# Kernel tuning notes

Hardware: AMD Instinct MI355X
Metric: run time of the kernel (lower is better)

The kernel has to match this reference:

```python
import jax, jax.numpy as jnp
import numpy as np

NUM_ORI = 16
DEGREE = 2
NUM_LAYERS = 2
LN_EPS = 1e-6


def ori_grid_s1(n):
    theta = jnp.linspace(0.0, 2.0 * jnp.pi, n + 1)[:-1]
    return jnp.stack([jnp.cos(theta), jnp.sin(theta)], axis=-1)  # (O, 2)


def poly_feats(z, degree):
    # PolynomialFeatures: [z, z*z outer, (z*z)*z outer ...] flattened
    feats = [z]
    p = z
    for _ in range(degree):
        p = (p[..., :, None] * z[..., None, :]).reshape(*z.shape[:-1], -1)
        feats.append(p)
    return jnp.concatenate(feats, axis=-1)


def basis_mlp(z, W1, b1, W2, b2):
    return jax.nn.gelu(jax.nn.gelu(z @ W1 + b1) @ W2 + b2)


def layer_norm(h, scale, bias):
    mu = h.mean(axis=-1, keepdims=True)
    var = ((h - mu) ** 2).mean(axis=-1, keepdims=True)
    return (h - mu) * jax.lax.rsqrt(var + LN_EPS) * scale + bias


def setup_inputs() -> dict:
    key = jax.random.key(0)
    ks = jax.random.split(key, 16)
    B, N, NIN, H, BD, WF, OUT, L = 1, 256, 3, 64, 32, 4, 3, NUM_LAYERS
    s = 0.05
    return {
        'pos': jax.random.normal(ks[0], (B, N, 2), jnp.float32),
        'x': jax.random.normal(ks[1], (B, N, NIN), jnp.float32),
        'skb_W1': jax.random.normal(ks[2], (14, H), jnp.float32) * s,
        'skb_b1': jnp.zeros((H,), jnp.float32),
        'skb_W2': jax.random.normal(ks[3], (H, BD), jnp.float32) * s,
        'skb_b2': jnp.zeros((BD,), jnp.float32),
        'rkb_W1': jax.random.normal(ks[4], (3, H), jnp.float32) * s,
        'rkb_b1': jnp.zeros((H,), jnp.float32),
        'rkb_W2': jax.random.normal(ks[5], (H, BD), jnp.float32) * s,
        'rkb_b2': jnp.zeros((BD,), jnp.float32),
        'emb_W': jax.random.normal(ks[6], (NIN, H), jnp.float32) * s,
        'conv_sW': jax.random.normal(ks[7], (L, BD, H), jnp.float32) * s,
        'conv_rW': jax.random.normal(ks[8], (L, BD, H), jnp.float32) * s,
        'conv_b': jnp.zeros((L, H), jnp.float32),
        'ln_scale': jnp.ones((L, H), jnp.float32),
        'ln_bias': jnp.zeros((L, H), jnp.float32),
        'lin1_W': jax.random.normal(ks[9], (L, H, WF * H), jnp.float32) * s,
        'lin1_b': jnp.zeros((L, WF * H), jnp.float32),
        'lin2_W': jax.random.normal(ks[10], (L, WF * H, H), jnp.float32) * s,
        'lin2_b': jnp.zeros((L, H), jnp.float32),
        'readout_W': jax.random.normal(ks[11], (H, OUT), jnp.float32) * s,
    }


def reference(pos, x, skb_W1, skb_b1, skb_W2, skb_b2, rkb_W1, rkb_b1, rkb_W2, rkb_b2,
              emb_W, conv_sW, conv_rW, conv_b, ln_scale, ln_bias,
              lin1_W, lin1_b, lin2_W, lin2_b, readout_W):
    ori = ori_grid_s1(NUM_ORI)  # (O, 2)
    # rel_pos: (B, n, m, 1, 2) -> broadcast against ori (O, 2)
    rel_pos = pos[:, None, :, None, :] - pos[:, :, None, None, :]
    inv1 = jnp.sum(rel_pos * ori[None, None, None, :, :], axis=-1, keepdims=True)  # (B,N,N,O,1)
    inv2 = jnp.linalg.norm(rel_pos - rel_pos * inv1, axis=-1, keepdims=True)       # (B,N,N,O,1)
    spatial_inv = jnp.concatenate([inv1, inv2], axis=-1)                            # (B,N,N,O,2)
    orient_inv = jnp.sum(ori[:, None, :] * ori[None, :, :], axis=-1, keepdims=True) # (O,O,1)

    kernel_basis = basis_mlp(poly_feats(spatial_inv, DEGREE), skb_W1, skb_b1, skb_W2, skb_b2)  # (B,N,N,O,BD)
    fiber_basis = basis_mlp(poly_feats(orient_inv, DEGREE), rkb_W1, rkb_b1, rkb_W2, rkb_b2)    # (O,O,BD)

    h = x @ emb_W                                  # (B,N,H)
    O = NUM_ORI
    h = jnp.broadcast_to(h[:, :, None, :], (h.shape[0], h.shape[1], O, h.shape[2]))  # (B,N,O,H)

    for i in range(NUM_LAYERS):
        inp = h
        sk = kernel_basis @ conv_sW[i]             # (B,N,N,O,H)
        rk = fiber_basis @ conv_rW[i]              # (O,O,H)
        c = jnp.einsum('bnoc,bmnoc->bmoc', h, sk)  # spatial aggregation
        c = jnp.einsum('bmoc,poc->bmpc', c, rk)    # orientation mixing
        c = c + conv_b[i]
        c = layer_norm(c, ln_scale[i], ln_bias[i])
        c = jax.nn.gelu(c @ lin1_W[i] + lin1_b[i]) @ lin2_W[i] + lin2_b[i]
        h = inp + c

    readout = h @ readout_W                        # (B,N,O,OUT)
    out_scalar = readout.mean(axis=-2)             # (B,N,OUT)
    out_scalar = jnp.sum(out_scalar, axis=1) / out_scalar.shape[1]  # global pool -> (B,OUT)
    return out_scalar
```

## Files before the change

kernel.cpp:

```cpp
#include <hip/hip_runtime.h>
#include <math.h>

#define NPTS 256
#define NORI 16
#define CH   64
#define BD   32
#define HID  64
#define STEP16 0.39269908169872414f

typedef __bf16 bf16x8 __attribute__((ext_vector_type(8)));
typedef float  f32x4  __attribute__((ext_vector_type(4)));

#define MFMA16(a, b, cc) __builtin_amdgcn_mfma_f32_16x16x32_bf16(a, b, cc, 0, 0, 0)

__device__ __forceinline__ float gelu_f(float x) {
    float x2 = x * x;
    float y2 = x * fmaf(0.07135481627f, x2, 1.5957691216f);
    float e = __expf(y2);
    return x - x * __builtin_amdgcn_rcpf(e + 1.0f);
}

__device__ __forceinline__ unsigned pk2(float x, float y) {
    union { __bf16 h[2]; unsigned u; } r;
    r.h[0] = (__bf16)x; r.h[1] = (__bf16)y;
    return r.u;
}

__device__ __forceinline__ void dev_prep(
    const float* __restrict__ skb_W1, const float* __restrict__ skb_W2,
    const float* __restrict__ conv_sW,
    __bf16* __restrict__ w1T, __bf16* __restrict__ w2T, __bf16* __restrict__ w2Tlo,
    __bf16* __restrict__ sWT, __bf16* __restrict__ sWTlo, int t)
{
    if (t < 64) {
        float f[9];
        f[0] = skb_W1[t];
        f[1] = skb_W1[64 + t];
        f[2] = skb_W1[128 + t];
        f[3] = skb_W1[192 + t] + skb_W1[256 + t];
        f[4] = skb_W1[320 + t];
        f[5] = skb_W1[384 + t];
        f[6] = skb_W1[448 + t] + skb_W1[512 + t] + skb_W1[640 + t];
        f[7] = skb_W1[576 + t] + skb_W1[704 + t] + skb_W1[768 + t];
        f[8] = skb_W1[832 + t];
#pragma unroll
        for (int k = 0; k < 9; ++k) {
            __bf16 hi = (__bf16)f[k];
            w1T[t * 32 + k]      = hi;
            w1T[t * 32 + 9 + k]  = (__bf16)(f[k] - (float)hi);
            w1T[t * 32 + 18 + k] = hi;
        }
#pragma unroll
        for (int k = 27; k < 32; ++k) w1T[t * 32 + k] = (__bf16)0.0f;
    }
    for (int i = t; i < 2048; i += 256) {
        int n = i >> 6, kk = i & 63;
        float v = skb_W2[kk * 32 + n];
        __bf16 hi = (__bf16)v;
        w2T[i]   = hi;
        w2Tlo[i] = (__bf16)(v - (float)hi);
    }
    for (int i = t; i < 4096; i += 256) {
        int ll = i >> 11, chh = (i >> 5) & 63, k = i & 31;
        float v = conv_sW[(ll * 32 + k) * 64 + chh];
        __bf16 hi = (__bf16)v;
        sWT[i]   = hi;
        sWTlo[i] = (__bf16)(v - (float)hi);
    }
}

__device__ __forceinline__ void dev_fiber(
    const float* __restrict__ rkb_W1, const float* __restrict__ rkb_b1,
    const float* __restrict__ rkb_W2, const float* __restrict__ rkb_b2,
    const float* __restrict__ conv_rW, float* __restrict__ rk, int p, int t)
{
    __shared__ float w1L[3 * 64], b1L[64], w2L[64 * 32], b2L[32];
    __shared__ float rwL[2 * 32 * 64];
    __shared__ float t1L[16 * 64];
    __shared__ float fbL[16 * 32];

    if (t < 192) w1L[t] = rkb_W1[t];
    if (t >= 192 && t < 256) b1L[t - 192] = rkb_b1[t - 192];
    for (int i = t; i < 2048; i += 256) w2L[i] = rkb_W2[i];
    if (t < 32) b2L[t] = rkb_b2[t];
    for (int i = t; i < 4096; i += 256) rwL[i] = conv_rW[i];
    __syncthreads();

    const int o = t & 15;
    const float cp = cosf(p * STEP16), sp = sinf(p * STEP16);
    const float co = cosf(o * STEP16), so = sinf(o * STEP16);
    const float s0 = cp * co + sp * so;
    const float m1 = s0 * s0, m2 = m1 * s0;

    {
        const int jg = t >> 4;
#pragma unroll
        for (int u = 0; u < 4; ++u) {
            const int j = jg * 4 + u;
            float a = b1L[j] + s0 * w1L[j] + m1 * w1L[64 + j] + m2 * w1L[128 + j];
            t1L[o * 64 + j] = gelu_f(a);
        }
    }
    __syncthreads();
    {
        const int kg = t >> 4;
#pragma unroll
        for (int kk = 0; kk < 2; ++kk) {
            const int k = kg + kk * 16;
            float a = b2L[k];
#pragma unroll
            for (int j = 0; j < 64; ++j) a += t1L[o * 64 + j] * w2L[j * 32 + k];
            fbL[o * 32 + k] = gelu_f(a);
        }
    }
    __syncthreads();
    {
        const int o2 = t >> 4;
        const int chg = (t & 15) * 4;
#pragma unroll
        for (int l = 0; l < 2; ++l) {
            f32x4 acc = {0.f, 0.f, 0.f, 0.f};
#pragma unroll
            for (int k = 0; k < 32; ++k) {
                const float fv = fbL[o2 * 32 + k];
                const f32x4 rv = *(const f32x4*)(rwL + (l * 32 + k) * 64 + chg);
                acc[0] = fmaf(fv, rv[0], acc[0]);
                acc[1] = fmaf(fv, rv[1], acc[1]);
                acc[2] = fmaf(fv, rv[2], acc[2]);
                acc[3] = fmaf(fv, rv[3], acc[3]);
            }
            *(f32x4*)(rk + (l * 256 + p * 16 + o2) * 64 + chg) = acc;
        }
    }
}

__global__ __launch_bounds__(256) void k_prep(
    const float* __restrict__ skb_W1, const float* __restrict__ skb_W2,
    const float* __restrict__ conv_sW,
    __bf16* __restrict__ w1T, __bf16* __restrict__ w2T, __bf16* __restrict__ w2Tlo,
    __bf16* __restrict__ sWT, __bf16* __restrict__ sWTlo)
{
    dev_prep(skb_W1, skb_W2, conv_sW, w1T, w2T, w2Tlo, sWT, sWTlo, threadIdx.x);
}

__global__ __launch_bounds__(256) void k_fiber2(
    const float* __restrict__ rkb_W1, const float* __restrict__ rkb_b1,
    const float* __restrict__ rkb_W2, const float* __restrict__ rkb_b2,
    const float* __restrict__ conv_rW, float* __restrict__ rk)
{
    dev_fiber(rkb_W1, rkb_b1, rkb_W2, rkb_b2, conv_rW, rk, blockIdx.x, threadIdx.x);
}

__global__ __launch_bounds__(256) void k_init(
    const float* __restrict__ x, const float* __restrict__ emb_W, float* __restrict__ h)
{
    int idx = blockIdx.x * 256 + threadIdx.x;
    int ch = idx & 63;
    int n  = idx >> 10;
    h[idx] = x[n * 3] * emb_W[ch] + x[n * 3 + 1] * emb_W[64 + ch] + x[n * 3 + 2] * emb_W[128 + ch];
}

__global__ __launch_bounds__(256) void k_setup(
    const float* __restrict__ x, const float* __restrict__ emb_W, float* __restrict__ h2,
    const float* __restrict__ rkb_W1, const float* __restrict__ rkb_b1,
    const float* __restrict__ rkb_W2, const float* __restrict__ rkb_b2,
    const float* __restrict__ conv_rW, float* __restrict__ rk,
    const float* __restrict__ skb_W1, const float* __restrict__ skb_W2,
    const float* __restrict__ conv_sW,
    __bf16* __restrict__ w1T, __bf16* __restrict__ w2T, __bf16* __restrict__ w2Tlo,
    __bf16* __restrict__ sWT, __bf16* __restrict__ sWTlo)
{
    const int b = blockIdx.x, t = threadIdx.x;
    if (b < 1024) {
        int idx = b * 256 + t;
        int ch = (idx >> 4) & 63;
        int n  = idx >> 10;
        h2[idx] = x[n * 3] * emb_W[ch] + x[n * 3 + 1] * emb_W[64 + ch]
                + x[n * 3 + 2] * emb_W[128 + ch];
    } else if (b < 1040) {
        dev_fiber(rkb_W1, rkb_b1, rkb_W2, rkb_b2, conv_rW, rk, b - 1024, t);
    } else {
        dev_prep(skb_W1, skb_W2, conv_sW, w1T, w2T, w2Tlo, sWT, sWTlo, t);
    }
}

__global__ __launch_bounds__(256) void k_kb2(
    const float* __restrict__ pos,
    const float* __restrict__ skb_b1, const float* __restrict__ skb_b2,
    const __bf16* __restrict__ w1T, const __bf16* __restrict__ w2T,
    const __bf16* __restrict__ w2Tlo, __bf16* __restrict__ kb_g)
{
    const int t = threadIdx.x;
    const int c = t & 15, qq = (t >> 4) & 3, w = t >> 6;
    const int pair = blockIdx.x >> 1, ohalf = blockIdx.x & 1;
    const int m0 = (pair >> 4) * 16, n0 = (pair & 15) * 16;

    bf16x8 w1B[4], w2A[2][2], w2Alo[2][2];
    float b1x[4][4], b2x[2][4];
#pragma unroll
    for (int ni = 0; ni < 4; ++ni) {
        w1B[ni] = *(const bf16x8*)(w1T + (ni * 16 + c) * 32 + qq * 8);
#pragma unroll
        for (int r = 0; r < 4; ++r) b1x[ni][r] = skb_b1[ni * 16 + qq * 4 + r];
    }
#pragma unroll
    for (int mk = 0; mk < 2; ++mk) {
#pragma unroll
        for (int ks = 0; ks < 2; ++ks) {
            w2A[mk][ks]   = *(const bf16x8*)(w2T   + (mk * 16 + c) * 64 + ks * 32 + qq * 8);
            w2Alo[mk][ks] = *(const bf16x8*)(w2Tlo + (mk * 16 + c) * 64 + ks * 32 + qq * 8);
        }
#pragma unroll
        for (int r = 0; r < 4; ++r) b2x[mk][r] = skb_b2[mk * 16 + qq * 4 + r];
    }

    const int n = n0 + c;
    const float pnx = pos[2 * n], pny = pos[2 * n + 1];
    float cosv[4], sinv[4];
#pragma unroll
    for (int oi = 0; oi < 4; ++oi) {
        float th = (float)(ohalf * 4 + oi) * STEP16;
        cosv[oi] = cosf(th); sinv[oi] = sinf(th);
    }
    const int s0lane = c + ((qq & 1) << 5);
    const int s1lane = s0lane + 16;
    const int selhi = qq >> 1;
    const f32x4 zf = {0.f, 0.f, 0.f, 0.f};

#pragma unroll 1
    for (int mi = 0; mi < 4; ++mi) {
        const int m = m0 + w * 4 + mi;
        const float dx = pnx - pos[2 * m];
        const float dy = pny - pos[2 * m + 1];
#pragma unroll
        for (int oi = 0; oi < 4; ++oi) {
            const int o = ohalf * 4 + oi;
            float a = dx * cosv[oi] + dy * sinv[oi];
            float vx = dx - dx * a, vy = dy - dy * a;
            float b = sqrtf(vx * vx + vy * vy);
            float mfv[9];
            mfv[0] = a; mfv[1] = b; mfv[2] = a * a; mfv[3] = a * b; mfv[4] = b * b;
            mfv[5] = mfv[2] * a; mfv[6] = mfv[2] * b; mfv[7] = mfv[3] * b; mfv[8] = mfv[4] * b;
            __bf16 mh[9], ml[9];
#pragma unroll
            for (int i = 0; i < 9; ++i) {
                mh[i] = (__bf16)mfv[i];
                ml[i] = (__bf16)(mfv[i] - (float)mh[i]);
            }
            bf16x8 mb;
            if (qq == 0) {
                mb[0]=mh[0]; mb[1]=mh[1]; mb[2]=mh[2]; mb[3]=mh[3];
                mb[4]=mh[4]; mb[5]=mh[5]; mb[6]=mh[6]; mb[7]=mh[7];
            } else if (qq == 1) {
                mb[0]=mh[8]; mb[1]=mh[0]; mb[2]=mh[1]; mb[3]=mh[2];
                mb[4]=mh[3]; mb[5]=mh[4]; mb[6]=mh[5]; mb[7]=mh[6];
            } else if (qq == 2) {
                mb[0]=mh[7]; mb[1]=mh[8]; mb[2]=ml[0]; mb[3]=ml[1];
                mb[4]=ml[2]; mb[5]=ml[3]; mb[6]=ml[4]; mb[7]=ml[5];
            } else {
                mb[0]=ml[6]; mb[1]=ml[7]; mb[2]=ml[8]; mb[3]=(__bf16)0.0f;
                mb[4]=(__bf16)0.0f; mb[5]=(__bf16)0.0f; mb[6]=(__bf16)0.0f; mb[7]=(__bf16)0.0f;
            }

            unsigned t1p[4][2];
#pragma unroll
            for (int ni = 0; ni < 4; ++ni) {
                f32x4 acc = MFMA16(w1B[ni], mb, zf);
                float g0 = gelu_f(acc[0] + b1x[ni][0]);
                float g1 = gelu_f(acc[1] + b1x[ni][1]);
                float g2 = gelu_f(acc[2] + b1x[ni][2]);
                float g3 = gelu_f(acc[3] + b1x[ni][3]);
                t1p[ni][0] = pk2(g0, g1);
                t1p[ni][1] = pk2(g2, g3);
            }

            bf16x8 B2[2];
#pragma unroll
            for (int ks = 0; ks < 2; ++ks) {
                const unsigned lo0 = t1p[ks * 2][0],     lo1 = t1p[ks * 2][1];
                const unsigned hi0 = t1p[ks * 2 + 1][0], hi1 = t1p[ks * 2 + 1][1];
                unsigned aL0 = (unsigned)__shfl((int)lo0, s0lane);
                unsigned aL1 = (unsigned)__shfl((int)lo1, s0lane);
                unsigned aL2 = (unsigned)__shfl((int)lo0, s1lane);
                unsigned aL3 = (unsigned)__shfl((int)lo1, s1lane);
                unsigned aH0 = (unsigned)__shfl((int)hi0, s0lane);
                unsigned aH1 = (unsigned)__shfl((int)hi1, s0lane);
                unsigned aH2 = (unsigned)__shfl((int)hi0, s1lane);
                unsigned aH3 = (unsigned)__shfl((int)hi1, s1lane);
                union { unsigned u[4]; bf16x8 v; } bu;
                bu.u[0] = selhi ? aH0 : aL0;
                bu.u[1] = selhi ? aH1 : aL1;
                bu.u[2] = selhi ? aH2 : aL2;
                bu.u[3] = selhi ? aH3 : aL3;
                B2[ks] = bu.v;
            }

            const size_t ptP = (size_t)((m * 256 + n) * 16 + o);
            const size_t ptM = (size_t)((n * 256 + m) * 16 + (o ^ 8));
#pragma unroll
            for (int mk = 0; mk < 2; ++mk) {
                f32x4 acc = MFMA16(w2A[mk][0], B2[0], zf);
                acc = MFMA16(w2A[mk][1], B2[1], acc);
                acc = MFMA16(w2Alo[mk][0], B2[0], acc);
                acc = MFMA16(w2Alo[mk][1], B2[1], acc);
                float g0 = gelu_f(acc[0] + b2x[mk][0]);
                float g1 = gelu_f(acc[1] + b2x[mk][1]);
                float g2 = gelu_f(acc[2] + b2x[mk][2]);
                float g3 = gelu_f(acc[3] + b2x[mk][3]);
                uint2 pv; pv.x = pk2(g0, g1); pv.y = pk2(g2, g3);
                const int off = mk * 32 + qq * 8;
                *(uint2*)((char*)kb_g + ptP * 64 + off) = pv;
                *(uint2*)((char*)kb_g + ptM * 64 + off) = pv;
            }
        }
    }
}

__global__ __launch_bounds__(512, 1) void k_conv(
    const __bf16* __restrict__ kb_g,
    const __bf16* __restrict__ sWT, const __bf16* __restrict__ sWTlo,
    const float* __restrict__ conv_b, const float* __restrict__ rkg,
    const float* __restrict__ ln_scale, const float* __restrict__ ln_bias,
    const float* __restrict__ lin1_W, const float* __restrict__ lin1_b,
    const float* __restrict__ lin2_W, const float* __restrict__ lin2_b,
    const float* __restrict__ h_in, float* __restrict__ h_out, int l)
{
    __shared__ __align__(16) unsigned char smem[57344];
    const int t = threadIdx.x;
    const int m = blockIdx.x;
    const int w = t >> 6, lane = t & 63;
    const int qq = lane >> 4, c = lane & 15;

    bf16x8 sWB[4], sWBlo[4];
#pragma unroll
    for (int ni = 0; ni < 4; ++ni) {
        sWB[ni]   = *(const bf16x8*)(sWT   + l * 2048 + (ni * 16 + c) * 32 + qq * 8);
        sWBlo[ni] = *(const bf16x8*)(sWTlo + l * 2048 + (ni * 16 + c) * 32 + qq * 8);
    }

    f32x4 cacc[4];
#pragma unroll
    for (int ni = 0; ni < 4; ++ni)
#pragma unroll
        for (int r = 0; r < 4; ++r) cacc[ni][r] = 0.f;

    const __bf16* kbm = kb_g + ((size_t)m << 17);

#pragma unroll 2
    for (int tile = 0; tile < 16; ++tile) {
#pragma unroll
        for (int mm = 0; mm < 2; ++mm) {
            const int mi = 2 * w + mm;
            const int n = tile * 16 + mi;
            bf16x8 aF = *(const bf16x8*)(kbm + (size_t)(tile * 256 + mi * 16 + c) * 32 + qq * 8);
#pragma unroll
            for (int ni = 0; ni < 4; ++ni) {
                f32x4 g3 = {0.f, 0.f, 0.f, 0.f};
                g3 = MFMA16(aF, sWB[ni], g3);
                g3 = MFMA16(aF, sWBlo[ni], g3);
                f32x4 hv = *(const f32x4*)(h_in + n * 1024 + (ni * 16 + c) * 16 + qq * 4);
#pragma unroll
                for (int r = 0; r < 4; ++r) cacc[ni][r] = fmaf(g3[r], hv[r], cacc[ni][r]);
            }
        }
    }

    {
        float* c1p = (float*)smem;
#pragma unroll
        for (int ni = 0; ni < 4; ++ni)
#pragma unroll
            for (int r = 0; r < 4; ++r)
                c1p[w * 1024 + (qq * 4 + r) * 64 + ni * 16 + c] = cacc[ni][r];
    }
    __syncthreads();
    {
        float* c1p = (float*)smem;
        float* c1r = (float*)(smem + 32768);
        for (int i = t; i < 1024; i += 512) {
            float s = 0.f;
#pragma unroll
            for (int ww = 0; ww < 8; ++ww) s += c1p[ww * 1024 + i];
            c1r[i] = s;
        }
    }
    __syncthreads();

    {
        float* c1r = (float*)(smem + 32768);
        float* cns = (float*)(smem + 36864);
        const int ch = lane;
        const float cb  = conv_b[l * 64 + ch];
        const float lsc = ln_scale[l * 64 + ch], lbi = ln_bias[l * 64 + ch];
#pragma unroll
        for (int pp = 0; pp < 2; ++pp) {
            const int p = w + pp * 8;
            const float* rkp = rkg + (l * 256 + p * 16) * 64 + ch;
            float s = cb;
#pragma unroll
            for (int o = 0; o < 16; ++o) s += c1r[o * 64 + ch] * rkp[o * 64];
            float red = s;
#pragma unroll
            for (int off = 32; off > 0; off >>= 1) red += __shfl_xor(red, off);
            float mu = red * (1.0f / 64.0f);
            float d = s - mu;
            float r2 = d * d;
#pragma unroll
            for (int off = 32; off > 0; off >>= 1) r2 += __shfl_xor(r2, off);
            cns[p * 64 + ch] = d * rsqrtf(r2 * (1.0f / 64.0f) + 1e-6f) * lsc + lbi;
        }
    }
    __syncthreads();

    {
        float* cns = (float*)(smem + 36864);
        float* usS = (float*)(smem + 40960);
        const int j = t & 255, half = t >> 8;
        const float* W1l = lin1_W + l * 64 * 256;
        const float bl1 = lin1_b[l * 256 + j];
        float ua[8];
#pragma unroll
        for (int pi = 0; pi < 8; ++pi) ua[pi] = bl1;
#pragma unroll 4
        for (int c2 = 0; c2 < 64; ++c2) {
            const float wv = W1l[c2 * 256 + j];
#pragma unroll
            for (int pi = 0; pi < 8; ++pi)
                ua[pi] = fmaf(cns[(half * 8 + pi) * 64 + c2], wv, ua[pi]);
        }
#pragma unroll
        for (int pi = 0; pi < 8; ++pi) usS[(half * 8 + pi) * 256 + j] = gelu_f(ua[pi]);
    }
    __syncthreads();

    {
        float* usS = (float*)(smem + 40960);
        const int ch2 = t & 63, pg = t >> 6;
        const float* W2l = lin2_W + l * 256 * 64;
        const float bl2 = lin2_b[l * 64 + ch2];
        float o0 = bl2, o1 = bl2;
#pragma unroll 4
        for (int j = 0; j < 256; ++j) {
            const float wv = W2l[j * 64 + ch2];
            o0 = fmaf(usS[pg * 256 + j], wv, o0);
            o1 = fmaf(usS[(pg + 8) * 256 + j], wv, o1);
        }
        const int i0 = m * 1024 + ch2 * 16 + pg;
        h_out[i0]     = h_in[i0]     + o0;
        h_out[i0 + 8] = h_in[i0 + 8] + o1;
    }
}

__global__ __launch_bounds__(512, 1) void k_layer2(
    const float* __restrict__ pos,
    const float* __restrict__ skb_b1, const float* __restrict__ skb_b2,
    const __bf16* __restrict__ w1T, const __bf16* __restrict__ w2T,
    const __bf16* __restrict__ w2Tlo,
    const __bf16* __restrict__ sWT, const __bf16* __restrict__ sWTlo,
    const float* __restrict__ conv_b, const float* __restrict__ rkg,
    const float* __restrict__ ln_scale, const float* __restrict__ ln_bias,
    const float* __restrict__ lin1_W, const float* __restrict__ lin1_b,
    const float* __restrict__ lin2_W, const float* __restrict__ lin2_b,
    const float* __restrict__ h_in, float* __restrict__ h_out, int l)
{
    __shared__ __align__(16) unsigned char smem[57344];
    const int t = threadIdx.x;
    const int m = blockIdx.x;
    const int w = t >> 6, lane = t & 63;
    const int qq = lane >> 4, c = lane & 15;

    bf16x8 w1B[4], sWB[4], sWBlo[4], w2B[2][2], w2Blo[2][2];
    float b1v[4], b2v[2];
#pragma unroll
    for (int ni = 0; ni < 4; ++ni) {
        w1B[ni]   = *(const bf16x8*)(w1T + (ni * 16 + c) * 32 + qq * 8);
        sWB[ni]   = *(const bf16x8*)(sWT   + l * 2048 + (ni * 16 + c) * 32 + qq * 8);
        sWBlo[ni] = *(const bf16x8*)(sWTlo + l * 2048 + (ni * 16 + c) * 32 + qq * 8);
        b1v[ni] = skb_b1[ni * 16 + c];
    }
#pragma unroll
    for (int nt = 0; nt < 2; ++nt) {
        b2v[nt] = skb_b2[nt * 16 + c];
#pragma unroll
        for (int ks = 0; ks < 2; ++ks) {
            w2B[nt][ks]   = *(const bf16x8*)(w2T   + (nt * 16 + c) * 64 + ks * 32 + qq * 8);
            w2Blo[nt][ks] = *(const bf16x8*)(w2Tlo + (nt * 16 + c) * 64 + ks * 32 + qq * 8);
        }
    }

    const float pmx = pos[2 * m], pmy = pos[2 * m + 1];
    float co_ = 0.f, so_ = 0.f;
    if (t < 256) { float th = (float)(t & 15) * STEP16; co_ = cosf(th); so_ = sinf(th); }

    f32x4 cacc[4];
#pragma unroll
    for (int ni = 0; ni < 4; ++ni)
#pragma unroll
        for (int r = 0; r < 4; ++r) cacc[ni][r] = 0.f;

#pragma unroll 1
    for (int tile = 0; tile < 16; ++tile) {
        if (t < 256) {
            const int n = tile * 16 + (t >> 4);
            float dx = pos[2 * n] - pmx, dy = pos[2 * n + 1] - pmy;
            float a = dx * co_ + dy * so_;
            float vx = dx - dx * a, vy = dy - dy * a;
            float b = sqrtf(vx * vx + vy * vy);
            float mf[9];
            mf[0] = a; mf[1] = b; mf[2] = a * a; mf[3] = a * b; mf[4] = b * b;
            mf[5] = mf[2] * a; mf[6] = mf[2] * b; mf[7] = mf[3] * b; mf[8] = mf[4] * b;
            __bf16 s[32];
#pragma unroll
            for (int i = 0; i < 9; ++i) {
                __bf16 hi = (__bf16)mf[i];
                s[i] = hi; s[9 + i] = hi;
                s[18 + i] = (__bf16)(mf[i] - (float)hi);
            }
#pragma unroll
            for (int i = 27; i < 32; ++i) s[i] = (__bf16)0.0f;
            unsigned char* rowp = smem + t * 64;
#pragma unroll
            for (int u = 0; u < 4; ++u) {
                bf16x8 vv;
#pragma unroll
                for (int j = 0; j < 8; ++j) vv[j] = s[u * 8 + j];
                *(bf16x8*)(rowp + ((u ^ (t & 3)) << 4)) = vv;
            }
        }
        __syncthreads();

#pragma unroll
        for (int mm = 0; mm < 2; ++mm) {
            const int row = (2 * w + mm) * 16 + c;
            bf16x8 aF = *(const bf16x8*)(smem + row * 64 + ((qq ^ (row & 3)) << 4));
#pragma unroll
            for (int ni = 0; ni < 4; ++ni) {
                f32x4 acc = {0.f, 0.f, 0.f, 0.f};
                acc = MFMA16(aF, w1B[ni], acc);
#pragma unroll
                for (int r = 0; r < 4; ++r) {
                    const int ro = (2 * w + mm) * 16 + qq * 4 + r;
                    float g = gelu_f(acc[r] + b1v[ni]);
                    const int chc = ni * 16 + c;
                    *(__bf16*)(smem + 16384 + ro * 128 + (((chc >> 3) ^ (ro & 7)) << 4)
                               + ((chc & 7) << 1)) = (__bf16)g;
                }
            }
        }
        __syncthreads();

#pragma unroll
        for (int mm = 0; mm < 2; ++mm) {
            const int row = (2 * w + mm) * 16 + c;
            bf16x8 a0 = *(const bf16x8*)(smem + 16384 + row * 128 + ((qq ^ (row & 7)) << 4));
            bf16x8 a1 = *(const bf16x8*)(smem + 16384 + row * 128 + (((4 + qq) ^ (row & 7)) << 4));
#pragma unroll
            for (int nt = 0; nt < 2; ++nt) {
                f32x4 acc = {0.f, 0.f, 0.f, 0.f};
                acc = MFMA16(a0, w2B[nt][0], acc);
                acc = MFMA16(a1, w2B[nt][1], acc);
                acc = MFMA16(a0, w2Blo[nt][0], acc);
                acc = MFMA16(a1, w2Blo[nt][1], acc);
#pragma unroll
                for (int r = 0; r < 4; ++r) {
                    const int ro = (2 * w + mm) * 16 + qq * 4 + r;
                    float g = gelu_f(acc[r] + b2v[nt]);
                    const int kc = nt * 16 + c;
                    *(__bf16*)(smem + ro * 64 + (((kc >> 3) ^ (ro & 3)) << 4)
                               + ((kc & 7) << 1)) = (__bf16)g;
                }
            }
        }
        __syncthreads();

#pragma unroll
        for (int mm = 0; mm < 2; ++mm) {
            const int mi = 2 * w + mm;
            const int row = mi * 16 + c;
            bf16x8 aF = *(const bf16x8*)(smem + row * 64 + ((qq ^ (row & 3)) << 4));
            const int nbase = (tile * 16 + mi) * 1024 + qq * 256;
#pragma unroll
            for (int ni = 0; ni < 4; ++ni) {
                f32x4 g3 = {0.f, 0.f, 0.f, 0.f};
                g3 = MFMA16(aF, sWB[ni], g3);
                g3 = MFMA16(aF, sWBlo[ni], g3);
#pragma unroll
                for (int r = 0; r < 4; ++r) {
                    float hv = h_in[nbase + r * 64 + ni * 16 + c];
                    cacc[ni][r] = fmaf(g3[r], hv, cacc[ni][r]);
                }
            }
        }
        __syncthreads();
    }

    {
        float* c1p = (float*)smem;
#pragma unroll
        for (int ni = 0; ni < 4; ++ni)
#pragma unroll
            for (int r = 0; r < 4; ++r)
                c1p[w * 1024 + (qq * 4 + r) * 64 + ni * 16 + c] = cacc[ni][r];
    }
    __syncthreads();
    {
        float* c1p = (float*)smem;
        float* c1r = (float*)(smem + 32768);
        for (int i = t; i < 1024; i += 512) {
            float s = 0.f;
#pragma unroll
            for (int ww = 0; ww < 8; ++ww) s += c1p[ww * 1024 + i];
            c1r[i] = s;
        }
    }
    __syncthreads();

    {
        float* c1r = (float*)(smem + 32768);
        float* cns = (float*)(smem + 36864);
        const int ch = lane;
        const float cb  = conv_b[l * 64 + ch];
        const float lsc = ln_scale[l * 64 + ch], lbi = ln_bias[l * 64 + ch];
#pragma unroll
        for (int pp = 0; pp < 2; ++pp) {
            const int p = w + pp * 8;
            const float* rkp = rkg + (l * 256 + p * 16) * 64 + ch;
            float s = cb;
#pragma unroll
            for (int o = 0; o < 16; ++o) s += c1r[o * 64 + ch] * rkp[o * 64];
            float red = s;
#pragma unroll
            for (int off = 32; off > 0; off >>= 1) red += __shfl_xor(red, off);
            float mu = red * (1.0f / 64.0f);
            float d = s - mu;
            float r2 = d * d;
#pragma unroll
            for (int off = 32; off > 0; off >>= 1) r2 += __shfl_xor(r2, off);
            cns[p * 64 + ch] = d * rsqrtf(r2 * (1.0f / 64.0f) + 1e-6f) * lsc + lbi;
        }
    }
    __syncthreads();

    {
        float* cns = (float*)(smem + 36864);
        float* usS = (float*)(smem + 40960);
        const int j = t & 255, half = t >> 8;
        const float* W1l = lin1_W + l * 64 * 256;
        const float bl1 = lin1_b[l * 256 + j];
        float ua[8];
#pragma unroll
        for (int pi = 0; pi < 8; ++pi) ua[pi] = bl1;
#pragma unroll 1
        for (int c2 = 0; c2 < 64; ++c2) {
            const float wv = W1l[c2 * 256 + j];
#pragma unroll
            for (int pi = 0; pi < 8; ++pi)
                ua[pi] = fmaf(cns[(half * 8 + pi) * 64 + c2], wv, ua[pi]);
        }
#pragma unroll
        for (int pi = 0; pi < 8; ++pi) usS[(half * 8 + pi) * 256 + j] = gelu_f(ua[pi]);
    }
    __syncthreads();

    {
        float* usS = (float*)(smem + 40960);
        const int ch2 = t & 63, pg = t >> 6;
        const float* W2l = lin2_W + l * 256 * 64;
        const float bl2 = lin2_b[l * 64 + ch2];
        float o0 = bl2, o1 = bl2;
#pragma unroll 2
        for (int j = 0; j < 256; ++j) {
            const float wv = W2l[j * 64 + ch2];
            o0 = fmaf(usS[pg * 256 + j], wv, o0);
            o1 = fmaf(usS[(pg + 8) * 256 + j], wv, o1);
        }
        const int i0 = (m * 16 + pg) * 64 + ch2;
        const int i1 = (m * 16 + pg + 8) * 64 + ch2;
        h_out[i0] = h_in[i0] + o0;
        h_out[i1] = h_in[i1] + o1;
    }
}

__global__ __launch_bounds__(256) void k_readout_part(
    const float* __restrict__ h, float* __restrict__ part16)
{
    __shared__ float part[4][64];
    const int t = threadIdx.x, b = blockIdx.x;
    const int c = t & 63, seg = t >> 6;
    float s = 0.f;
    const int r0 = b * 256 + seg * 64;
    for (int r = r0; r < r0 + 64; ++r) s += h[r * 64 + c];
    part[seg][c] = s;
    __syncthreads();
    if (t < 64) part16[b * 64 + t] = part[0][t] + part[1][t] + part[2][t] + part[3][t];
}

__global__ __launch_bounds__(256) void k_readout_part2(
    const float* __restrict__ h, float* __restrict__ part16)
{
    const int t = threadIdx.x, b = blockIdx.x;
    const int ch = t >> 2, oq = t & 3;
    float s = 0.f;
#pragma unroll
    for (int nn = 0; nn < 16; ++nn) {
        const int n = b * 16 + nn;
        f32x4 v = *(const f32x4*)(h + n * 1024 + ch * 16 + oq * 4);
        s += (v[0] + v[1]) + (v[2] + v[3]);
    }
    s += __shfl_xor(s, 1);
    s += __shfl_xor(s, 2);
    if (oq == 0) part16[b * 64 + ch] = s;
}

__global__ __launch_bounds__(64) void k_readout_final(
    const float* __restrict__ part16, const float* __restrict__ rW, float* __restrict__ out)
{
    __shared__ float hbar[64];
    const int t = threadIdx.x;
    float s = 0.f;
#pragma unroll
    for (int b = 0; b < 16; ++b) s += part16[b * 64 + t];
    hbar[t] = s * (1.0f / 4096.0f);
    __syncthreads();
    if (t < 3) {
        float s2 = 0.f;
#pragma unroll
        for (int k = 0; k < 64; ++k) s2 += hbar[k] * rW[k * 3 + t];
        out[t] = s2;
    }
}

extern "C" void kernel_launch(void* const* d_in, const int* in_sizes, int n_in,
                              void* d_out, int out_size, void* d_ws, size_t ws_size,
                              hipStream_t stream)
{
    const float* pos      = (const float*)d_in[0];
    const float* x        = (const float*)d_in[1];
    const float* skb_W1   = (const float*)d_in[2];
    const float* skb_b1   = (const float*)d_in[3];
    const float* skb_W2   = (const float*)d_in[4];
    const float* skb_b2   = (const float*)d_in[5];
    const float* rkb_W1   = (const float*)d_in[6];
    const float* rkb_b1   = (const float*)d_in[7];
    const float* rkb_W2   = (const float*)d_in[8];
    const float* rkb_b2   = (const float*)d_in[9];
    const float* emb_W    = (const float*)d_in[10];
    const float* conv_sW  = (const float*)d_in[11];
    const float* conv_rW  = (const float*)d_in[12];
    const float* conv_b   = (const float*)d_in[13];
    const float* ln_scale = (const float*)d_in[14];
    const float* ln_bias  = (const float*)d_in[15];
    const float* lin1_W   = (const float*)d_in[16];
    const float* lin1_b   = (const float*)d_in[17];
    const float* lin2_W   = (const float*)d_in[18];
    const float* lin2_b   = (const float*)d_in[19];
    const float* readout_W= (const float*)d_in[20];
    float* out = (float*)d_out;

    unsigned char* ws = (unsigned char*)d_ws;
    float*  h_a    = (float*)(ws);
    float*  h_b    = (float*)(ws + 1048576);
    float*  rkw    = (float*)(ws + 2097152);
    __bf16* w1T    = (__bf16*)(ws + 2228224);
    __bf16* w2T    = (__bf16*)(ws + 2232320);
    __bf16* w2Tlo  = (__bf16*)(ws + 2236416);
    __bf16* sWT    = (__bf16*)(ws + 2240512);
    __bf16* sWTlo  = (__bf16*)(ws + 2248704);
    float*  part16 = (float*)(ws + 2256896);
    __bf16* kb_g   = (__bf16*)(ws + 2260992);

    const bool fast = (ws_size >= 2260992ull + 67108864ull);

    if (fast) {
        k_setup<<<1041, 256, 0, stream>>>(x, emb_W, h_a,
                                          rkb_W1, rkb_b1, rkb_W2, rkb_b2, conv_rW, rkw,
                                          skb_W1, skb_W2, conv_sW,
                                          w1T, w2T, w2Tlo, sWT, sWTlo);
        k_kb2<<<512, 256, 0, stream>>>(pos, skb_b1, skb_b2, w1T, w2T, w2Tlo, kb_g);
        k_conv<<<256, 512, 0, stream>>>(kb_g, sWT, sWTlo, conv_b, rkw,
                                        ln_scale, ln_bias, lin1_W, lin1_b,
                                        lin2_W, lin2_b, h_a, h_b, 0);
        k_conv<<<256, 512, 0, stream>>>(kb_g, sWT, sWTlo, conv_b, rkw,
                                        ln_scale, ln_bias, lin1_W, lin1_b,
                                        lin2_W, lin2_b, h_b, h_a, 1);
        k_readout_part2<<<16, 256, 0, stream>>>(h_a, part16);
        k_readout_final<<<1, 64, 0, stream>>>(part16, readout_W, out);
    } else {
        k_prep<<<1, 256, 0, stream>>>(skb_W1, skb_W2, conv_sW, w1T, w2T, w2Tlo, sWT, sWTlo);
        k_fiber2<<<16, 256, 0, stream>>>(rkb_W1, rkb_b1, rkb_W2, rkb_b2, conv_rW, rkw);
        k_init<<<1024, 256, 0, stream>>>(x, emb_W, h_a);
        k_layer2<<<256, 512, 0, stream>>>(pos, skb_b1, skb_b2, w1T, w2T, w2Tlo, sWT, sWTlo,
                                          conv_b, rkw, ln_scale, ln_bias, lin1_W, lin1_b,
                                          lin2_W, lin2_b, h_a, h_b, 0);
        k_layer2<<<256, 512, 0, stream>>>(pos, skb_b1, skb_b2, w1T, w2T, w2Tlo, sWT, sWTlo,
                                          conv_b, rkw, ln_scale, ln_bias, lin1_W, lin1_b,
                                          lin2_W, lin2_b, h_b, h_a, 1);
        k_readout_part<<<16, 256, 0, stream>>>(h_a, part16);
        k_readout_final<<<1, 64, 0, stream>>>(part16, readout_W, out);
    }
}
```

Baseline: 157.2 us.

## Double block size of conv kernel and software-prefetch next tile operands

```diff
diff --git a/kernel.cpp b/kernel.cpp
--- a/kernel.cpp
+++ b/kernel.cpp
@@ -316,7 +316,7 @@
     }
 }
 
-__global__ __launch_bounds__(512, 1) void k_conv(
+__global__ __launch_bounds__(1024) void k_conv2(
     const __bf16* __restrict__ kb_g,
     const __bf16* __restrict__ sWT, const __bf16* __restrict__ sWTlo,
     const float* __restrict__ conv_b, const float* __restrict__ rkg,
@@ -325,11 +325,12 @@
     const float* __restrict__ lin2_W, const float* __restrict__ lin2_b,
     const float* __restrict__ h_in, float* __restrict__ h_out, int l)
 {
-    __shared__ __align__(16) unsigned char smem[57344];
+    __shared__ __align__(16) unsigned char smem[90112];
     const int t = threadIdx.x;
     const int m = blockIdx.x;
     const int w = t >> 6, lane = t & 63;
     const int qq = lane >> 4, c = lane & 15;
+    const f32x4 zf = {0.f, 0.f, 0.f, 0.f};
 
     bf16x8 sWB[4], sWBlo[4];
 #pragma unroll
@@ -345,24 +346,48 @@
         for (int r = 0; r < 4; ++r) cacc[ni][r] = 0.f;
 
     const __bf16* kbm = kb_g + ((size_t)m << 17);
-
-#pragma unroll 2
+    const __bf16* abase = kbm + (size_t)(w * 16 + c) * 32 + qq * 8;
+
+    bf16x8 aF = *(const bf16x8*)(abase);
+    f32x4 hc0, hc1, hc2, hc3;
+    {
+        const float* hp = h_in + (w) * 1024 + c * 16 + qq * 4;
+        hc0 = *(const f32x4*)(hp);
+        hc1 = *(const f32x4*)(hp + 256);
+        hc2 = *(const f32x4*)(hp + 512);
+        hc3 = *(const f32x4*)(hp + 768);
+    }
+
+#pragma unroll 1
     for (int tile = 0; tile < 16; ++tile) {
-#pragma unroll
-        for (int mm = 0; mm < 2; ++mm) {
-            const int mi = 2 * w + mm;
-            const int n = tile * 16 + mi;
-            bf16x8 aF = *(const bf16x8*)(kbm + (size_t)(tile * 256 + mi * 16 + c) * 32 + qq * 8);
-#pragma unroll
-            for (int ni = 0; ni < 4; ++ni) {
-                f32x4 g3 = {0.f, 0.f, 0.f, 0.f};
-                g3 = MFMA16(aF, sWB[ni], g3);
-                g3 = MFMA16(aF, sWBlo[ni], g3);
-                f32x4 hv = *(const f32x4*)(h_in + n * 1024 + (ni * 16 + c) * 16 + qq * 4);
-#pragma unroll
-                for (int r = 0; r < 4; ++r) cacc[ni][r] = fmaf(g3[r], hv[r], cacc[ni][r]);
-            }
-        }
+        const int tn = (tile < 15) ? tile + 1 : 15;
+        bf16x8 aN = *(const bf16x8*)(abase + (size_t)tn * 8192);
+        const float* hpn = h_in + (tn * 16 + w) * 1024 + c * 16 + qq * 4;
+        f32x4 hn0 = *(const f32x4*)(hpn);
+        f32x4 hn1 = *(const f32x4*)(hpn + 256);
+        f32x4 hn2 = *(const f32x4*)(hpn + 512);
+        f32x4 hn3 = *(const f32x4*)(hpn + 768);
+
+        f32x4 g;
+        g = MFMA16(aF, sWB[0], zf);
+        g = MFMA16(aF, sWBlo[0], g);
+#pragma unroll
+        for (int r = 0; r < 4; ++r) cacc[0][r] = fmaf(g[r], hc0[r], cacc[0][r]);
+        g = MFMA16(aF, sWB[1], zf);
+        g = MFMA16(aF, sWBlo[1], g);
+#pragma unroll
+        for (int r = 0; r < 4; ++r) cacc[1][r] = fmaf(g[r], hc1[r], cacc[1][r]);
+        g = MFMA16(aF, sWB[2], zf);
+        g = MFMA16(aF, sWBlo[2], g);
+#pragma unroll
+        for (int r = 0; r < 4; ++r) cacc[2][r] = fmaf(g[r], hc2[r], cacc[2][r]);
+        g = MFMA16(aF, sWB[3], zf);
+        g = MFMA16(aF, sWBlo[3], g);
+#pragma unroll
+        for (int r = 0; r < 4; ++r) cacc[3][r] = fmaf(g[r], hc3[r], cacc[3][r]);
+
+        aF = aN;
+        hc0 = hn0; hc1 = hn1; hc2 = hn2; hc3 = hn3;
     }
 
     {
@@ -376,78 +401,67 @@
     __syncthreads();
     {
         float* c1p = (float*)smem;
-        float* c1r = (float*)(smem + 32768);
-        for (int i = t; i < 1024; i += 512) {
-            float s = 0.f;
-#pragma unroll
-            for (int ww = 0; ww < 8; ++ww) s += c1p[ww * 1024 + i];
-            c1r[i] = s;
-        }
-    }
-    __syncthreads();
-
-    {
-        float* c1r = (float*)(smem + 32768);
-        float* cns = (float*)(smem + 36864);
+        float* c1r = (float*)(smem + 65536);
+        float s = 0.f;
+#pragma unroll
+        for (int ww = 0; ww < 16; ++ww) s += c1p[ww * 1024 + t];
+        c1r[t] = s;
+    }
+    __syncthreads();
+
+    {
+        float* c1r = (float*)(smem + 65536);
+        float* cns = (float*)(smem + 69632);
         const int ch = lane;
         const float cb  = conv_b[l * 64 + ch];
         const float lsc = ln_scale[l * 64 + ch], lbi = ln_bias[l * 64 + ch];
-#pragma unroll
-        for (int pp = 0; pp < 2; ++pp) {
-            const int p = w + pp * 8;
-            const float* rkp = rkg + (l * 256 + p * 16) * 64 + ch;
-            float s = cb;
-#pragma unroll
-            for (int o = 0; o < 16; ++o) s += c1r[o * 64 + ch] * rkp[o * 64];
-            float red = s;
-#pragma unroll
-            for (int off = 32; off > 0; off >>= 1) red += __shfl_xor(red, off);
-            float mu = red * (1.0f / 64.0f);
-            float d = s - mu;
-            float r2 = d * d;
-#pragma unroll
-            for (int off = 32; off > 0; off >>= 1) r2 += __shfl_xor(r2, off);
-            cns[p * 64 + ch] = d * rsqrtf(r2 * (1.0f / 64.0f) + 1e-6f) * lsc + lbi;
-        }
-    }
-    __syncthreads();
-
-    {
-        float* cns = (float*)(smem + 36864);
-        float* usS = (float*)(smem + 40960);
-        const int j = t & 255, half = t >> 8;
+        const float* rkp = rkg + (l * 256 + w * 16) * 64 + ch;
+        float s = cb;
+#pragma unroll
+        for (int o = 0; o < 16; ++o) s += c1r[o * 64 + ch] * rkp[o * 64];
+        float red = s;
+#pragma unroll
+        for (int off = 32; off > 0; off >>= 1) red += __shfl_xor(red, off);
+        float mu = red * (1.0f / 64.0f);
+        float d = s - mu;
+        float r2 = d * d;
+#pragma unroll
+        for (int off = 32; off > 0; off >>= 1) r2 += __shfl_xor(r2, off);
+        cns[w * 64 + ch] = d * rsqrtf(r2 * (1.0f / 64.0f) + 1e-6f) * lsc + lbi;
+    }
+    __syncthreads();
+
+    {
+        float* cns = (float*)(smem + 69632);
+        float* usS = (float*)(smem + 73728);
+        const int j = t & 255, q4 = t >> 8;
         const float* W1l = lin1_W + l * 64 * 256;
         const float bl1 = lin1_b[l * 256 + j];
-        float ua[8];
-#pragma unroll
-        for (int pi = 0; pi < 8; ++pi) ua[pi] = bl1;
+        float ua[4];
+#pragma unroll
+        for (int pi = 0; pi < 4; ++pi) ua[pi] = bl1;
 #pragma unroll 4
         for (int c2 = 0; c2 < 64; ++c2) {
             const float wv = W1l[c2 * 256 + j];
 #pragma unroll
-            for (int pi = 0; pi < 8; ++pi)
-                ua[pi] = fmaf(cns[(half * 8 + pi) * 64 + c2], wv, ua[pi]);
-        }
-#pragma unroll
-        for (int pi = 0; pi < 8; ++pi) usS[(half * 8 + pi) * 256 + j] = gelu_f(ua[pi]);
-    }
-    __syncthreads();
-
-    {
-        float* usS = (float*)(smem + 40960);
+            for (int pi = 0; pi < 4; ++pi)
+                ua[pi] = fmaf(cns[(q4 * 4 + pi) * 64 + c2], wv, ua[pi]);
+        }
+#pragma unroll
+        for (int pi = 0; pi < 4; ++pi) usS[(q4 * 4 + pi) * 256 + j] = gelu_f(ua[pi]);
+    }
+    __syncthreads();
+
+    {
+        float* usS = (float*)(smem + 73728);
         const int ch2 = t & 63, pg = t >> 6;
         const float* W2l = lin2_W + l * 256 * 64;
-        const float bl2 = lin2_b[l * 64 + ch2];
-        float o0 = bl2, o1 = bl2;
+        float o0 = lin2_b[l * 64 + ch2];
 #pragma unroll 4
-        for (int j = 0; j < 256; ++j) {
-            const float wv = W2l[j * 64 + ch2];
-            o0 = fmaf(usS[pg * 256 + j], wv, o0);
-            o1 = fmaf(usS[(pg + 8) * 256 + j], wv, o1);
-        }
+        for (int j = 0; j < 256; ++j)
+            o0 = fmaf(usS[pg * 256 + j], W2l[j * 64 + ch2], o0);
         const int i0 = m * 1024 + ch2 * 16 + pg;
-        h_out[i0]     = h_in[i0]     + o0;
-        h_out[i0 + 8] = h_in[i0 + 8] + o1;
+        h_out[i0] = h_in[i0] + o0;
     }
 }
 
@@ -777,12 +791,12 @@
                                           skb_W1, skb_W2, conv_sW,
                                           w1T, w2T, w2Tlo, sWT, sWTlo);
         k_kb2<<<512, 256, 0, stream>>>(pos, skb_b1, skb_b2, w1T, w2T, w2Tlo, kb_g);
-        k_conv<<<256, 512, 0, stream>>>(kb_g, sWT, sWTlo, conv_b, rkw,
-                                        ln_scale, ln_bias, lin1_W, lin1_b,
-                                        lin2_W, lin2_b, h_a, h_b, 0);
-        k_conv<<<256, 512, 0, stream>>>(kb_g, sWT, sWTlo, conv_b, rkw,
-                                        ln_scale, ln_bias, lin1_W, lin1_b,
-                                        lin2_W, lin2_b, h_b, h_a, 1);
+        k_conv2<<<256, 1024, 0, stream>>>(kb_g, sWT, sWTlo, conv_b, rkw,
+                                          ln_scale, ln_bias, lin1_W, lin1_b,
+                                          lin2_W, lin2_b, h_a, h_b, 0);
+        k_conv2<<<256, 1024, 0, stream>>>(kb_g, sWT, sWTlo, conv_b, rkw,
+                                          ln_scale, ln_bias, lin1_W, lin1_b,
+                                          lin2_W, lin2_b, h_b, h_a, 1);
         k_readout_part2<<<16, 256, 0, stream>>>(h_a, part16);
         k_readout_final<<<1, 64, 0, stream>>>(part16, readout_W, out);
     } else {
```

Result: faster. 146.3 us (-6.9%).

## Fuse kernel-basis MLP into conv kernel, recompute per layer instead of materialising

Applied to the files above, without the earlier changes.

```diff
diff --git a/kernel.cpp b/kernel.cpp
--- a/kernel.cpp
+++ b/kernel.cpp
@@ -27,9 +27,10 @@
 }
 
 __device__ __forceinline__ void dev_prep(
-    const float* __restrict__ skb_W1, const float* __restrict__ skb_W2,
-    const float* __restrict__ conv_sW,
+    const float* __restrict__ skb_W1, const float* __restrict__ skb_b1,
+    const float* __restrict__ skb_W2, const float* __restrict__ conv_sW,
     __bf16* __restrict__ w1T, __bf16* __restrict__ w2T, __bf16* __restrict__ w2Tlo,
+    __bf16* __restrict__ w2Tp, __bf16* __restrict__ w2Tplo,
     __bf16* __restrict__ sWT, __bf16* __restrict__ sWTlo, int t)
 {
     if (t < 64) {
@@ -52,6 +53,10 @@
         }
 #pragma unroll
         for (int k = 27; k < 32; ++k) w1T[t * 32 + k] = (__bf16)0.0f;
+        float bv = skb_b1[t];
+        __bf16 bh = (__bf16)bv;
+        w1T[t * 32 + 27] = bh;
+        w1T[t * 32 + 28] = (__bf16)(bv - (float)bh);
     }
     for (int i = t; i < 2048; i += 256) {
         int n = i >> 6, kk = i & 63;
@@ -59,6 +64,13 @@
         __bf16 hi = (__bf16)v;
         w2T[i]   = hi;
         w2Tlo[i] = (__bf16)(v - (float)hi);
+        int row = i >> 6, ch = i & 63;
+        int mk = row >> 4, ii = row & 15;
+        int kp = 8 * (ii >> 2) + 4 * mk + (ii & 3);
+        float vp = skb_W2[ch * 32 + kp];
+        __bf16 hp = (__bf16)vp;
+        w2Tp[i]   = hp;
+        w2Tplo[i] = (__bf16)(vp - (float)hp);
     }
     for (int i = t; i < 4096; i += 256) {
         int ll = i >> 11, chh = (i >> 5) & 63, k = i & 31;
@@ -135,12 +147,14 @@
 }
 
 __global__ __launch_bounds__(256) void k_prep(
-    const float* __restrict__ skb_W1, const float* __restrict__ skb_W2,
-    const float* __restrict__ conv_sW,
+    const float* __restrict__ skb_W1, const float* __restrict__ skb_b1,
+    const float* __restrict__ skb_W2, const float* __restrict__ conv_sW,
     __bf16* __restrict__ w1T, __bf16* __restrict__ w2T, __bf16* __restrict__ w2Tlo,
+    __bf16* __restrict__ w2Tp, __bf16* __restrict__ w2Tplo,
     __bf16* __restrict__ sWT, __bf16* __restrict__ sWTlo)
 {
-    dev_prep(skb_W1, skb_W2, conv_sW, w1T, w2T, w2Tlo, sWT, sWTlo, threadIdx.x);
+    dev_prep(skb_W1, skb_b1, skb_W2, conv_sW, w1T, w2T, w2Tlo, w2Tp, w2Tplo,
+             sWT, sWTlo, threadIdx.x);
 }
 
 __global__ __launch_bounds__(256) void k_fiber2(
@@ -165,9 +179,10 @@
     const float* __restrict__ rkb_W1, const float* __restrict__ rkb_b1,
     const float* __restrict__ rkb_W2, const float* __restrict__ rkb_b2,
     const float* __restrict__ conv_rW, float* __restrict__ rk,
-    const float* __restrict__ skb_W1, const float* __restrict__ skb_W2,
-    const float* __restrict__ conv_sW,
+    const float* __restrict__ skb_W1, const float* __restrict__ skb_b1,
+    const float* __restrict__ skb_W2, const float* __restrict__ conv_sW,
     __bf16* __restrict__ w1T, __bf16* __restrict__ w2T, __bf16* __restrict__ w2Tlo,
+    __bf16* __restrict__ w2Tp, __bf16* __restrict__ w2Tplo,
     __bf16* __restrict__ sWT, __bf16* __restrict__ sWTlo)
 {
     const int b = blockIdx.x, t = threadIdx.x;
@@ -180,62 +195,67 @@
     } else if (b < 1040) {
         dev_fiber(rkb_W1, rkb_b1, rkb_W2, rkb_b2, conv_rW, rk, b - 1024, t);
     } else {
-        dev_prep(skb_W1, skb_W2, conv_sW, w1T, w2T, w2Tlo, sWT, sWTlo, t);
-    }
-}
-
-__global__ __launch_bounds__(256) void k_kb2(
-    const float* __restrict__ pos,
-    const float* __restrict__ skb_b1, const float* __restrict__ skb_b2,
-    const __bf16* __restrict__ w1T, const __bf16* __restrict__ w2T,
-    const __bf16* __restrict__ w2Tlo, __bf16* __restrict__ kb_g)
-{
+        dev_prep(skb_W1, skb_b1, skb_W2, conv_sW, w1T, w2T, w2Tlo, w2Tp, w2Tplo,
+                 sWT, sWTlo, t);
+    }
+}
+
+__global__ __launch_bounds__(512, 1) void k_fused(
+    const float* __restrict__ pos, const float* __restrict__ skb_b2,
+    const __bf16* __restrict__ w1T,
+    const __bf16* __restrict__ w2Tp, const __bf16* __restrict__ w2Tplo,
+    const __bf16* __restrict__ sWT, const __bf16* __restrict__ sWTlo,
+    const float* __restrict__ conv_b, const float* __restrict__ rkg,
+    const float* __restrict__ ln_scale, const float* __restrict__ ln_bias,
+    const float* __restrict__ lin1_W, const float* __restrict__ lin1_b,
+    const float* __restrict__ lin2_W, const float* __restrict__ lin2_b,
+    const float* __restrict__ h_in, float* __restrict__ h_out, int l)
+{
+    __shared__ __align__(16) unsigned char smem[57344];
     const int t = threadIdx.x;
-    const int c = t & 15, qq = (t >> 4) & 3, w = t >> 6;
-    const int pair = blockIdx.x >> 1, ohalf = blockIdx.x & 1;
-    const int m0 = (pair >> 4) * 16, n0 = (pair & 15) * 16;
-
-    bf16x8 w1B[4], w2A[2][2], w2Alo[2][2];
-    float b1x[4][4], b2x[2][4];
+    const int m = blockIdx.x;
+    const int w = t >> 6, lane = t & 63;
+    const int qq = lane >> 4, c = lane & 15;
+    const f32x4 zf = {0.f, 0.f, 0.f, 0.f};
+
+    bf16x8 w1B[4], w2A[2][2], w2Alo[2][2], sWB[4], sWBlo[4];
+    float b2x[2][4];
 #pragma unroll
     for (int ni = 0; ni < 4; ++ni) {
-        w1B[ni] = *(const bf16x8*)(w1T + (ni * 16 + c) * 32 + qq * 8);
-#pragma unroll
-        for (int r = 0; r < 4; ++r) b1x[ni][r] = skb_b1[ni * 16 + qq * 4 + r];
+        w1B[ni]   = *(const bf16x8*)(w1T + (ni * 16 + c) * 32 + qq * 8);
+        sWB[ni]   = *(const bf16x8*)(sWT   + l * 2048 + (ni * 16 + c) * 32 + qq * 8);
+        sWBlo[ni] = *(const bf16x8*)(sWTlo + l * 2048 + (ni * 16 + c) * 32 + qq * 8);
     }
 #pragma unroll
     for (int mk = 0; mk < 2; ++mk) {
 #pragma unroll
         for (int ks = 0; ks < 2; ++ks) {
-            w2A[mk][ks]   = *(const bf16x8*)(w2T   + (mk * 16 + c) * 64 + ks * 32 + qq * 8);
-            w2Alo[mk][ks] = *(const bf16x8*)(w2Tlo + (mk * 16 + c) * 64 + ks * 32 + qq * 8);
-        }
-#pragma unroll
-        for (int r = 0; r < 4; ++r) b2x[mk][r] = skb_b2[mk * 16 + qq * 4 + r];
-    }
-
-    const int n = n0 + c;
-    const float pnx = pos[2 * n], pny = pos[2 * n + 1];
-    float cosv[4], sinv[4];
-#pragma unroll
-    for (int oi = 0; oi < 4; ++oi) {
-        float th = (float)(ohalf * 4 + oi) * STEP16;
-        cosv[oi] = cosf(th); sinv[oi] = sinf(th);
-    }
+            w2A[mk][ks]   = *(const bf16x8*)(w2Tp   + (mk * 16 + c) * 64 + ks * 32 + qq * 8);
+            w2Alo[mk][ks] = *(const bf16x8*)(w2Tplo + (mk * 16 + c) * 64 + ks * 32 + qq * 8);
+        }
+#pragma unroll
+        for (int r = 0; r < 4; ++r) b2x[mk][r] = skb_b2[qq * 8 + mk * 4 + r];
+    }
+
+    const float pmx = pos[2 * m], pmy = pos[2 * m + 1];
+    const float co_ = cosf((float)c * STEP16), so_ = sinf((float)c * STEP16);
     const int s0lane = c + ((qq & 1) << 5);
     const int s1lane = s0lane + 16;
     const int selhi = qq >> 1;
-    const f32x4 zf = {0.f, 0.f, 0.f, 0.f};
+
+    f32x4 cacc[4];
+#pragma unroll
+    for (int ni = 0; ni < 4; ++ni)
+#pragma unroll
+        for (int r = 0; r < 4; ++r) cacc[ni][r] = 0.f;
 
 #pragma unroll 1
-    for (int mi = 0; mi < 4; ++mi) {
-        const int m = m0 + w * 4 + mi;
-        const float dx = pnx - pos[2 * m];
-        const float dy = pny - pos[2 * m + 1];
-#pragma unroll
-        for (int oi = 0; oi < 4; ++oi) {
-            const int o = ohalf * 4 + oi;
-            float a = dx * cosv[oi] + dy * sinv[oi];
+    for (int tile = 0; tile < 16; ++tile) {
+#pragma unroll
+        for (int mm = 0; mm < 2; ++mm) {
+            const int n = tile * 16 + 2 * w + mm;
+            const float dx = pos[2 * n] - pmx, dy = pos[2 * n + 1] - pmy;
+            float a = dx * co_ + dy * so_;
             float vx = dx - dx * a, vy = dy - dy * a;
             float b = sqrtf(vx * vx + vy * vy);
             float mfv[9];
@@ -258,20 +278,16 @@
                 mb[0]=mh[7]; mb[1]=mh[8]; mb[2]=ml[0]; mb[3]=ml[1];
                 mb[4]=ml[2]; mb[5]=ml[3]; mb[6]=ml[4]; mb[7]=ml[5];
             } else {
-                mb[0]=ml[6]; mb[1]=ml[7]; mb[2]=ml[8]; mb[3]=(__bf16)0.0f;
-                mb[4]=(__bf16)0.0f; mb[5]=(__bf16)0.0f; mb[6]=(__bf16)0.0f; mb[7]=(__bf16)0.0f;
+                mb[0]=ml[6]; mb[1]=ml[7]; mb[2]=ml[8]; mb[3]=(__bf16)1.0f;
+                mb[4]=(__bf16)1.0f; mb[5]=(__bf16)0.0f; mb[6]=(__bf16)0.0f; mb[7]=(__bf16)0.0f;
             }
 
             unsigned t1p[4][2];
 #pragma unroll
             for (int ni = 0; ni < 4; ++ni) {
                 f32x4 acc = MFMA16(w1B[ni], mb, zf);
-                float g0 = gelu_f(acc[0] + b1x[ni][0]);
-                float g1 = gelu_f(acc[1] + b1x[ni][1]);
-                float g2 = gelu_f(acc[2] + b1x[ni][2]);
-                float g3 = gelu_f(acc[3] + b1x[ni][3]);
-                t1p[ni][0] = pk2(g0, g1);
-                t1p[ni][1] = pk2(g2, g3);
+                t1p[ni][0] = pk2(gelu_f(acc[0]), gelu_f(acc[1]));
+                t1p[ni][1] = pk2(gelu_f(acc[2]), gelu_f(acc[3]));
             }
 
             bf16x8 B2[2];
@@ -295,70 +311,24 @@
                 B2[ks] = bu.v;
             }
 
-            const size_t ptP = (size_t)((m * 256 + n) * 16 + o);
-            const size_t ptM = (size_t)((n * 256 + m) * 16 + (o ^ 8));
+            bf16x8 kbA;
 #pragma unroll
             for (int mk = 0; mk < 2; ++mk) {
                 f32x4 acc = MFMA16(w2A[mk][0], B2[0], zf);
                 acc = MFMA16(w2A[mk][1], B2[1], acc);
                 acc = MFMA16(w2Alo[mk][0], B2[0], acc);
                 acc = MFMA16(w2Alo[mk][1], B2[1], acc);
-                float g0 = gelu_f(acc[0] + b2x[mk][0]);
-                float g1 = gelu_f(acc[1] + b2x[mk][1]);
-                float g2 = gelu_f(acc[2] + b2x[mk][2]);
-                float g3 = gelu_f(acc[3] + b2x[mk][3]);
-                uint2 pv; pv.x = pk2(g0, g1); pv.y = pk2(g2, g3);
-                const int off = mk * 32 + qq * 8;
-                *(uint2*)((char*)kb_g + ptP * 64 + off) = pv;
-                *(uint2*)((char*)kb_g + ptM * 64 + off) = pv;
-            }
-        }
-    }
-}
-
-__global__ __launch_bounds__(512, 1) void k_conv(
-    const __bf16* __restrict__ kb_g,
-    const __bf16* __restrict__ sWT, const __bf16* __restrict__ sWTlo,
-    const float* __restrict__ conv_b, const float* __restrict__ rkg,
-    const float* __restrict__ ln_scale, const float* __restrict__ ln_bias,
-    const float* __restrict__ lin1_W, const float* __restrict__ lin1_b,
-    const float* __restrict__ lin2_W, const float* __restrict__ lin2_b,
-    const float* __restrict__ h_in, float* __restrict__ h_out, int l)
-{
-    __shared__ __align__(16) unsigned char smem[57344];
-    const int t = threadIdx.x;
-    const int m = blockIdx.x;
-    const int w = t >> 6, lane = t & 63;
-    const int qq = lane >> 4, c = lane & 15;
-
-    bf16x8 sWB[4], sWBlo[4];
-#pragma unroll
-    for (int ni = 0; ni < 4; ++ni) {
-        sWB[ni]   = *(const bf16x8*)(sWT   + l * 2048 + (ni * 16 + c) * 32 + qq * 8);
-        sWBlo[ni] = *(const bf16x8*)(sWTlo + l * 2048 + (ni * 16 + c) * 32 + qq * 8);
-    }
-
-    f32x4 cacc[4];
-#pragma unroll
-    for (int ni = 0; ni < 4; ++ni)
-#pragma unroll
-        for (int r = 0; r < 4; ++r) cacc[ni][r] = 0.f;
-
-    const __bf16* kbm = kb_g + ((size_t)m << 17);
-
-#pragma unroll 2
-    for (int tile = 0; tile < 16; ++tile) {
-#pragma unroll
-        for (int mm = 0; mm < 2; ++mm) {
-            const int mi = 2 * w + mm;
-            const int n = tile * 16 + mi;
-            bf16x8 aF = *(const bf16x8*)(kbm + (size_t)(tile * 256 + mi * 16 + c) * 32 + qq * 8);
+#pragma unroll
+                for (int r = 0; r < 4; ++r)
+                    kbA[mk * 4 + r] = (__bf16)gelu_f(acc[r] + b2x[mk][r]);
+            }
+
+            const float* hp = h_in + n * 1024 + c * 16 + qq * 4;
 #pragma unroll
             for (int ni = 0; ni < 4; ++ni) {
-                f32x4 g3 = {0.f, 0.f, 0.f, 0.f};
-                g3 = MFMA16(aF, sWB[ni], g3);
-                g3 = MFMA16(aF, sWBlo[ni], g3);
-                f32x4 hv = *(const f32x4*)(h_in + n * 1024 + (ni * 16 + c) * 16 + qq * 4);
+                f32x4 g3 = MFMA16(kbA, sWB[ni], zf);
+                g3 = MFMA16(kbA, sWBlo[ni], g3);
+                f32x4 hv = *(const f32x4*)(hp + ni * 256);
 #pragma unroll
                 for (int r = 0; r < 4; ++r) cacc[ni][r] = fmaf(g3[r], hv[r], cacc[ni][r]);
             }
@@ -767,26 +737,27 @@
     __bf16* sWT    = (__bf16*)(ws + 2240512);
     __bf16* sWTlo  = (__bf16*)(ws + 2248704);
     float*  part16 = (float*)(ws + 2256896);
-    __bf16* kb_g   = (__bf16*)(ws + 2260992);
-
-    const bool fast = (ws_size >= 2260992ull + 67108864ull);
+    __bf16* w2Tp   = (__bf16*)(ws + 2260992);
+    __bf16* w2Tplo = (__bf16*)(ws + 2265088);
+
+    const bool fast = (ws_size >= 2269184ull);
 
     if (fast) {
         k_setup<<<1041, 256, 0, stream>>>(x, emb_W, h_a,
                                           rkb_W1, rkb_b1, rkb_W2, rkb_b2, conv_rW, rkw,
-                                          skb_W1, skb_W2, conv_sW,
-                                          w1T, w2T, w2Tlo, sWT, sWTlo);
-        k_kb2<<<512, 256, 0, stream>>>(pos, skb_b1, skb_b2, w1T, w2T, w2Tlo, kb_g);
-        k_conv<<<256, 512, 0, stream>>>(kb_g, sWT, sWTlo, conv_b, rkw,
-                                        ln_scale, ln_bias, lin1_W, lin1_b,
-                                        lin2_W, lin2_b, h_a, h_b, 0);
-        k_conv<<<256, 512, 0, stream>>>(kb_g, sWT, sWTlo, conv_b, rkw,
-                                        ln_scale, ln_bias, lin1_W, lin1_b,
-                                        lin2_W, lin2_b, h_b, h_a, 1);
+                                          skb_W1, skb_b1, skb_W2, conv_sW,
+                                          w1T, w2T, w2Tlo, w2Tp, w2Tplo, sWT, sWTlo);
+        k_fused<<<256, 512, 0, stream>>>(pos, skb_b2, w1T, w2Tp, w2Tplo, sWT, sWTlo,
+                                         conv_b, rkw, ln_scale, ln_bias, lin1_W, lin1_b,
+                                         lin2_W, lin2_b, h_a, h_b, 0);
+        k_fused<<<256, 512, 0, stream>>>(pos, skb_b2, w1T, w2Tp, w2Tplo, sWT, sWTlo,
+                                         conv_b, rkw, ln_scale, ln_bias, lin1_W, lin1_b,
+                                         lin2_W, lin2_b, h_b, h_a, 1);
         k_readout_part2<<<16, 256, 0, stream>>>(h_a, part16);
         k_readout_final<<<1, 64, 0, stream>>>(part16, readout_W, out);
     } else {
-        k_prep<<<1, 256, 0, stream>>>(skb_W1, skb_W2, conv_sW, w1T, w2T, w2Tlo, sWT, sWTlo);
+        k_prep<<<1, 256, 0, stream>>>(skb_W1, skb_b1, skb_W2, conv_sW,
+                                      w1T, w2T, w2Tlo, w2Tp, w2Tplo, sWT, sWTlo);
         k_fiber2<<<16, 256, 0, stream>>>(rkb_W1, rkb_b1, rkb_W2, rkb_b2, conv_rW, rkw);
         k_init<<<1024, 256, 0, stream>>>(x, emb_W, h_a);
         k_layer2<<<256, 512, 0, stream>>>(pos, skb_b1, skb_b2, w1T, w2T, w2Tlo, sWT, sWTlo,
```

Measured after the change: 165.5 us. +5.3%, slower.
